# Performance work log

Hardware: AMD Instinct MI355X
Metric: run time of the kernel (lower is better)

The kernel has to match this reference:

```python
import jax, jax.numpy as jnp
import numpy as np

GRID_NUM = 3  # pykan 'grid' (number of intervals)
K = 3         # spline order

def bspline_basis(x, grid, k):
    # Cox-de Boor recursion, matching pykan B_batch with a shared extended grid.
    # x: (N, Din); grid: (G,) extended grid with G = GRID_NUM + 2*k + 1
    x = x[..., None]  # (N, Din, 1)
    B = ((x >= grid[:-1]) & (x < grid[1:])).astype(x.dtype)  # (N, Din, G-1)
    for p in range(1, k + 1):
        left = (x - grid[:-(p + 1)]) / (grid[p:-1] - grid[:-(p + 1)])
        right = (grid[p + 1:] - x) / (grid[p + 1:] - grid[1:-p])
        B = left * B[..., :-1] + right * B[..., 1:]
    return B  # (N, Din, GRID_NUM + k)

def setup_inputs() -> dict:
    key = jax.random.key(0)
    k1, k2, k3 = jax.random.split(key, 3)
    Bsz, S, Din, Dout = 4, 2048, 768, 768
    x = jax.random.normal(k1, (Bsz, S, Din), dtype=jnp.float32)
    # noise-scale-like init for spline coefficients (noise_scale=0.1)
    coef = (0.1 / GRID_NUM) * jax.random.normal(k2, (Dout, Din, GRID_NUM + K), dtype=jnp.float32)
    inv_sqrt_in = np.float32(1.0 / np.sqrt(Din))
    scale_base = inv_sqrt_in + 0.1 * inv_sqrt_in * jax.random.normal(k3, (Dout, Din), dtype=jnp.float32)
    scale_sp = jnp.ones((Dout, Din), dtype=jnp.float32)
    bias = jnp.zeros((Dout,), dtype=jnp.float32)
    return {"x": x, "coef": coef, "scale_base": scale_base, "scale_sp": scale_sp, "bias": bias}

def reference(x, coef, scale_base, scale_sp, bias):
    # x: (B, S, Din) -> flatten tokens as the original module does
    Bsz, S, Din = x.shape
    xf = x.reshape(-1, Din)  # (N, Din)
    # extended grid: linspace(-1,1,GRID_NUM+1) extended by K points each side (h = 2/GRID_NUM)
    h = 2.0 / GRID_NUM
    grid = jnp.arange(-K, GRID_NUM + K + 1, dtype=x.dtype) * h - 1.0  # (GRID_NUM + 2K + 1,)
    basis = bspline_basis(xf, grid, K)  # (N, Din, GRID_NUM+K)
    # per-edge activation: scale_base*silu(x) + scale_sp*spline(x); mask==1; symbolic branch==0
    base = jax.nn.silu(xf) @ scale_base.T  # (N, Dout)
    spline = jnp.einsum('nim,oim->no', basis, scale_sp[:, :, None] * coef)  # (N, Dout)
    out = base + spline + bias  # bias from pykan biases[l].weight
    return out.reshape(Bsz, S, -1)
```

## Files before the change

kernel.cpp:

```cpp
#include <hip/hip_runtime.h>
#include <hip/hip_bf16.h>


typedef _Float16 f16;
typedef __attribute__((ext_vector_type(8))) _Float16 f16x8;
typedef __attribute__((ext_vector_type(4))) float f32x4;

#define NTOK 8192
#define DIN 768
#define DOUT 768
#define KAUG 5376
#define BM 128
#define BN 96
#define BK 32
#define KSPLIT 2
#define KSEG (KAUG / KSPLIT)
#define KT (KSEG / BK)

#define A_BLOCKS 3072
#define W_BLOCKS 288
#define Z_BLOCKS 1536

typedef __attribute__((address_space(1))) void gvoid;
typedef __attribute__((address_space(3))) void lvoid;

__global__ __launch_bounds__(256) void build_all(const float* __restrict__ x,
                                                 const float* __restrict__ sb,
                                                 const float* __restrict__ ssp,
                                                 const float* __restrict__ coef,
                                                 f16* __restrict__ Aa,
                                                 f16* __restrict__ Wa,
                                                 float* __restrict__ out) {
  const int b = blockIdx.x;
  if (b < A_BLOCKS) {
    const int t = b * 256 + threadIdx.x;
    const int n = t / 96;
    const int i8 = (t - n * 96) * 8;

    const float4* xp = (const float4*)(x + (size_t)n * DIN + i8);
    float4 va = xp[0], vb = xp[1];
    float xv[8] = {va.x, va.y, va.z, va.w, vb.x, vb.y, vb.z, vb.w};

    f16x8 sil;
    f16x8 Bv[6];
#pragma unroll
    for (int e = 0; e < 8; ++e) {
      const float v = xv[e];
      sil[e] = (f16)__fdividef(v, 1.0f + __expf(-v));

      const float s = (v + 1.0f) * 1.5f + 3.0f;
      const float fi = floorf(s);
      const int i0 = (int)fi;
      const float u = s - fi;
      const float um = 1.0f - u;
      const float u2 = u * u, u3 = u2 * u;
      const float w0 = um * um * um * (1.0f / 6.0f);
      const float w1 = (3.0f * u3 - 6.0f * u2 + 4.0f) * (1.0f / 6.0f);
      const float w2 = (-3.0f * u3 + 3.0f * u2 + 3.0f * u + 1.0f) * (1.0f / 6.0f);
      const float w3 = u3 * (1.0f / 6.0f);
#pragma unroll
      for (int m = 0; m < 6; ++m) {
        const int d = m - i0 + 3;
        float w = (d == 0) ? w0 : (d == 1) ? w1 : (d == 2) ? w2 : (d == 3) ? w3 : 0.0f;
        Bv[m][e] = (f16)w;
      }
    }

    const size_t base = (size_t)n * KAUG + i8;
    *(f16x8*)&Aa[base] = sil;
#pragma unroll
    for (int m = 0; m < 6; ++m) *(f16x8*)&Aa[base + (size_t)(m + 1) * DIN] = Bv[m];
  } else if (b < A_BLOCKS + W_BLOCKS) {
    const int t = (b - A_BLOCKS) * 256 + threadIdx.x;
    const int o = t / 96;
    const int i8 = (t - o * 96) * 8;
    const size_t idx = (size_t)o * DIN + i8;

    float bb[8], sp[8], cf[48];
    *(float4*)&bb[0] = ((const float4*)(sb + idx))[0];
    *(float4*)&bb[4] = ((const float4*)(sb + idx))[1];
    *(float4*)&sp[0] = ((const float4*)(ssp + idx))[0];
    *(float4*)&sp[4] = ((const float4*)(ssp + idx))[1];
#pragma unroll
    for (int v = 0; v < 12; ++v) *(float4*)&cf[v * 4] = ((const float4*)(coef + idx * 6))[v];

    f16x8 ch0;
    f16x8 chm[6];
#pragma unroll
    for (int e = 0; e < 8; ++e) {
      ch0[e] = (f16)bb[e];
#pragma unroll
      for (int m = 0; m < 6; ++m) chm[m][e] = (f16)(sp[e] * cf[e * 6 + m]);
    }
    const size_t base = (size_t)o * KAUG + i8;
    *(f16x8*)&Wa[base] = ch0;
#pragma unroll
    for (int m = 0; m < 6; ++m) *(f16x8*)&Wa[base + (size_t)(m + 1) * DIN] = chm[m];
  } else {
    const int t = (b - A_BLOCKS - W_BLOCKS) * 256 + threadIdx.x;
    float4* o4 = (float4*)out;
    const float4 z = {0.f, 0.f, 0.f, 0.f};
#pragma unroll
    for (int s = 0; s < 4; ++s) o4[(size_t)t * 4 + s] = z;
  }
}

__global__ __launch_bounds__(256, 4) void kan_gemm(const f16* __restrict__ A,
                                                   const f16* __restrict__ W,
                                                   const float* __restrict__ bias,
                                                   float* __restrict__ out) {
  __shared__ alignas(16) f16 As[2][BM * BK];
  __shared__ alignas(16) f16 Bs[2][BN * BK];

  const int bid = blockIdx.x;
  const int xcd = bid & 7;
  const int slot = bid >> 3;
  const int mb = ((slot & 7) << 3) + xcd;
  const int rest = slot >> 3;
  const int nb = rest & 7;
  const int ks = rest >> 3;
  const int m0 = mb * BM;
  const int n0 = nb * BN;
  const size_t kbase = (size_t)ks * KSEG;

  const int tid = threadIdx.x;
  const int wave = tid >> 6;
  const int lane = tid & 63;
  const int wm = (wave >> 1) * 64;
  const int wn = (wave & 1) * 48;
  const int r = lane & 15;
  const int q = lane >> 4;

  f32x4 acc[4][3] = {};

  const int c0 = wave * 64 + lane;
  const int rowA0 = c0 >> 2, kq0 = c0 & 3;
  const int c1 = c0 + 256;
  const int rowA1 = c1 >> 2, kq1 = c1 & 3;

  const f16* gA0 = A + (size_t)(m0 + rowA0) * KAUG + kbase + kq0 * 8;
  const f16* gA1 = A + (size_t)(m0 + rowA1) * KAUG + kbase + kq1 * 8;
  const f16* gB0 = W + (size_t)(n0 + rowA0) * KAUG + kbase + kq0 * 8;
  const f16* gB1 = W + (size_t)(n0 + rowA1) * KAUG + kbase + kq1 * 8;

  const int woff = wave * 512;

  auto stage = [&](int buf, int kt) {
    const int koff = kt * BK;
    __builtin_amdgcn_global_load_lds((gvoid*)(gA0 + koff), (lvoid*)(&As[buf][woff]), 16, 0, 0);
    __builtin_amdgcn_global_load_lds((gvoid*)(gA1 + koff), (lvoid*)(&As[buf][woff + 2048]), 16, 0, 0);
    __builtin_amdgcn_global_load_lds((gvoid*)(gB0 + koff), (lvoid*)(&Bs[buf][woff]), 16, 0, 0);
    if (wave < 2)
      __builtin_amdgcn_global_load_lds((gvoid*)(gB1 + koff), (lvoid*)(&Bs[buf][woff + 2048]), 16, 0, 0);
  };

  stage(0, 0);

  for (int kt = 0; kt < KT; ++kt) {
    const int buf = kt & 1;
    __syncthreads();
    if (kt + 1 < KT) stage(buf ^ 1, kt + 1);

    f16x8 af[4], bf[3];
#pragma unroll
    for (int mi = 0; mi < 4; ++mi)
      af[mi] = *(const f16x8*)&As[buf][(wm + mi * 16 + r) * BK + q * 8];
#pragma unroll
    for (int ni = 0; ni < 3; ++ni)
      bf[ni] = *(const f16x8*)&Bs[buf][(wn + ni * 16 + r) * BK + q * 8];
#pragma unroll
    for (int mi = 0; mi < 4; ++mi)
#pragma unroll
      for (int ni = 0; ni < 3; ++ni)
        acc[mi][ni] =
            __builtin_amdgcn_mfma_f32_16x16x32_f16(af[mi], bf[ni], acc[mi][ni], 0, 0, 0);
  }

#pragma unroll
  for (int ni = 0; ni < 3; ++ni) {
    const int gcol = n0 + wn + ni * 16 + r;
    const float badd = (ks == 0) ? bias[gcol] : 0.0f;
#pragma unroll
    for (int mi = 0; mi < 4; ++mi) {
#pragma unroll
      for (int rg = 0; rg < 4; ++rg) {
        const int grow = m0 + wm + mi * 16 + q * 4 + rg;
        atomicAdd(&out[(size_t)grow * DOUT + gcol], acc[mi][ni][rg] + badd);
      }
    }
  }
}

extern "C" void kernel_launch(void* const* d_in, const int* in_sizes, int n_in,
                              void* d_out, int out_size, void* d_ws, size_t ws_size,
                              hipStream_t stream) {
  const float* x = (const float*)d_in[0];
  const float* coef = (const float*)d_in[1];
  const float* scale_base = (const float*)d_in[2];
  const float* scale_sp = (const float*)d_in[3];
  const float* bias = (const float*)d_in[4];
  float* out = (float*)d_out;

  f16* Aa = (f16*)d_ws;
  f16* Wa = (f16*)((char*)d_ws + (size_t)NTOK * KAUG * 2);

  build_all<<<A_BLOCKS + W_BLOCKS + Z_BLOCKS, 256, 0, stream>>>(x, scale_base, scale_sp,
                                                                coef, Aa, Wa, out);
  kan_gemm<<<8 * 128, 256, 0, stream>>>(Aa, Wa, bias, out);
}
```

Before: 228.6 us.

## Fuse activation basis construction into GEMM, drop materialized A matrix

Basis and SiLU features are now computed on the fly from x inside the GEMM and written straight to LDS, so the large fp16 augmented A matrix no longer goes out to global memory and back. The GEMM tile grows to 128x128, and the K split changes to two halves over the input dimension, each covering all seven feature channels. This removes most of the global memory traffic but puts the per-element spline math on the GEMM critical path. The loop is single-buffered with several syncs per iteration and 2 blocks per CU, so load/compute overlap and occupancy may drop.

```diff
diff --git a/kernel.cpp b/kernel.cpp
--- a/kernel.cpp
+++ b/kernel.cpp
@@ -11,43 +11,118 @@
 #define DOUT 768
 #define KAUG 5376
 #define BM 128
-#define BN 96
-#define BK 32
-#define KSPLIT 2
-#define KSEG (KAUG / KSPLIT)
-#define KT (KSEG / BK)
-
-#define A_BLOCKS 3072
+#define BN 128
+#define IB 32
+#define ISEG 384
+#define NIB 12
+
+#define ASTRIDE 40
+#define ASLICE (128 * ASTRIDE)
+#define BSLICE (128 * 32)
+
 #define W_BLOCKS 288
 #define Z_BLOCKS 1536
 
 typedef __attribute__((address_space(1))) void gvoid;
 typedef __attribute__((address_space(3))) void lvoid;
 
-__global__ __launch_bounds__(256) void build_all(const float* __restrict__ x,
-                                                 const float* __restrict__ sb,
-                                                 const float* __restrict__ ssp,
-                                                 const float* __restrict__ coef,
-                                                 f16* __restrict__ Aa,
-                                                 f16* __restrict__ Wa,
-                                                 float* __restrict__ out) {
+__global__ __launch_bounds__(256) void prep(const float* __restrict__ sb,
+                                            const float* __restrict__ ssp,
+                                            const float* __restrict__ coef,
+                                            f16* __restrict__ Wa,
+                                            float* __restrict__ out) {
   const int b = blockIdx.x;
-  if (b < A_BLOCKS) {
+  if (b < W_BLOCKS) {
     const int t = b * 256 + threadIdx.x;
-    const int n = t / 96;
-    const int i8 = (t - n * 96) * 8;
-
-    const float4* xp = (const float4*)(x + (size_t)n * DIN + i8);
-    float4 va = xp[0], vb = xp[1];
-    float xv[8] = {va.x, va.y, va.z, va.w, vb.x, vb.y, vb.z, vb.w};
-
-    f16x8 sil;
-    f16x8 Bv[6];
+    const int o = t / 96;
+    const int i8 = (t - o * 96) * 8;
+    const size_t idx = (size_t)o * DIN + i8;
+
+    float bb[8], sp[8], cf[48];
+    *(float4*)&bb[0] = ((const float4*)(sb + idx))[0];
+    *(float4*)&bb[4] = ((const float4*)(sb + idx))[1];
+    *(float4*)&sp[0] = ((const float4*)(ssp + idx))[0];
+    *(float4*)&sp[4] = ((const float4*)(ssp + idx))[1];
+#pragma unroll
+    for (int v = 0; v < 12; ++v) *(float4*)&cf[v * 4] = ((const float4*)(coef + idx * 6))[v];
+
+    f16x8 ch0, chm[6];
 #pragma unroll
     for (int e = 0; e < 8; ++e) {
+      ch0[e] = (f16)bb[e];
+#pragma unroll
+      for (int m = 0; m < 6; ++m) chm[m][e] = (f16)(sp[e] * cf[e * 6 + m]);
+    }
+    const size_t base = (size_t)o * KAUG + i8;
+    *(f16x8*)&Wa[base] = ch0;
+#pragma unroll
+    for (int m = 0; m < 6; ++m) *(f16x8*)&Wa[base + (size_t)(m + 1) * DIN] = chm[m];
+  } else {
+    const int t = (b - W_BLOCKS) * 256 + threadIdx.x;
+    float4* o4 = (float4*)out;
+    const float4 z = {0.f, 0.f, 0.f, 0.f};
+#pragma unroll
+    for (int s = 0; s < 4; ++s) o4[(size_t)t * 4 + s] = z;
+  }
+}
+
+__global__ __launch_bounds__(256, 2) void kan_fused(const float* __restrict__ x,
+                                                    const f16* __restrict__ Wa,
+                                                    const float* __restrict__ bias,
+                                                    float* __restrict__ out) {
+  __shared__ alignas(16) f16 As[4 * ASLICE];
+  __shared__ alignas(16) f16 Bs[4 * BSLICE];
+
+  const int bid = blockIdx.x;
+  const int xcd = bid & 7;
+  const int slot = bid >> 3;
+  const int mb = ((slot & 7) << 3) + xcd;
+  const int rest = slot >> 3;
+  const int nb = rest % 6;
+  const int ks = rest / 6;
+  const int m0 = mb * BM;
+  const int n0 = nb * BN;
+  const int ibase = ks * ISEG;
+
+  const int tid = threadIdx.x;
+  const int wave = tid >> 6;
+  const int lane = tid & 63;
+  const int wm = (wave >> 1) * 64;
+  const int wn = (wave & 1) * 64;
+  const int r = lane & 15;
+  const int q = lane >> 4;
+
+  const int xrow = tid >> 1;
+  const int ih = (tid & 1) * 16;
+  const float* xptr = x + (size_t)(m0 + xrow) * DIN + ibase + ih;
+  const int arow_off = xrow * ASTRIDE + ih;
+
+  const int c0 = wave * 64 + lane;
+  const int c1 = c0 + 256;
+  const f16* gB0 = Wa + (size_t)(n0 + (c0 >> 2)) * KAUG + ibase + (c0 & 3) * 8;
+  const f16* gB1 = Wa + (size_t)(n0 + (c1 >> 2)) * KAUG + ibase + (c1 & 3) * 8;
+  const int boff = wave * 512;
+
+  f32x4 acc[4][4] = {};
+
+  float4 xa[4];
+  xa[0] = ((const float4*)xptr)[0];
+  xa[1] = ((const float4*)xptr)[1];
+  xa[2] = ((const float4*)xptr)[2];
+  xa[3] = ((const float4*)xptr)[3];
+
+  for (int it = 0; it < NIB; ++it) {
+    float xv[16];
+    *(float4*)&xv[0] = xa[0];
+    *(float4*)&xv[4] = xa[1];
+    *(float4*)&xv[8] = xa[2];
+    *(float4*)&xv[12] = xa[3];
+
+    f16x8 chv[7][2];
+#pragma unroll
+    for (int e = 0; e < 16; ++e) {
       const float v = xv[e];
-      sil[e] = (f16)__fdividef(v, 1.0f + __expf(-v));
-
+      const float sil = __fdividef(v, 1.0f + __expf(-v));
       const float s = (v + 1.0f) * 1.5f + 3.0f;
       const float fi = floorf(s);
       const int i0 = (int)fi;
@@ -58,126 +133,79 @@
       const float w1 = (3.0f * u3 - 6.0f * u2 + 4.0f) * (1.0f / 6.0f);
       const float w2 = (-3.0f * u3 + 3.0f * u2 + 3.0f * u + 1.0f) * (1.0f / 6.0f);
       const float w3 = u3 * (1.0f / 6.0f);
+      chv[0][e >> 3][e & 7] = (f16)sil;
 #pragma unroll
       for (int m = 0; m < 6; ++m) {
         const int d = m - i0 + 3;
-        float w = (d == 0) ? w0 : (d == 1) ? w1 : (d == 2) ? w2 : (d == 3) ? w3 : 0.0f;
-        Bv[m][e] = (f16)w;
+        const float w = (d == 0) ? w0 : (d == 1) ? w1 : (d == 2) ? w2 : (d == 3) ? w3 : 0.0f;
+        chv[1 + m][e >> 3][e & 7] = (f16)w;
       }
     }
 
-    const size_t base = (size_t)n * KAUG + i8;
-    *(f16x8*)&Aa[base] = sil;
-#pragma unroll
-    for (int m = 0; m < 6; ++m) *(f16x8*)&Aa[base + (size_t)(m + 1) * DIN] = Bv[m];
-  } else if (b < A_BLOCKS + W_BLOCKS) {
-    const int t = (b - A_BLOCKS) * 256 + threadIdx.x;
-    const int o = t / 96;
-    const int i8 = (t - o * 96) * 8;
-    const size_t idx = (size_t)o * DIN + i8;
-
-    float bb[8], sp[8], cf[48];
-    *(float4*)&bb[0] = ((const float4*)(sb + idx))[0];
-    *(float4*)&bb[4] = ((const float4*)(sb + idx))[1];
-    *(float4*)&sp[0] = ((const float4*)(ssp + idx))[0];
-    *(float4*)&sp[4] = ((const float4*)(ssp + idx))[1];
-#pragma unroll
-    for (int v = 0; v < 12; ++v) *(float4*)&cf[v * 4] = ((const float4*)(coef + idx * 6))[v];
-
-    f16x8 ch0;
-    f16x8 chm[6];
-#pragma unroll
-    for (int e = 0; e < 8; ++e) {
-      ch0[e] = (f16)bb[e];
-#pragma unroll
-      for (int m = 0; m < 6; ++m) chm[m][e] = (f16)(sp[e] * cf[e * 6 + m]);
-    }
-    const size_t base = (size_t)o * KAUG + i8;
-    *(f16x8*)&Wa[base] = ch0;
-#pragma unroll
-    for (int m = 0; m < 6; ++m) *(f16x8*)&Wa[base + (size_t)(m + 1) * DIN] = chm[m];
-  } else {
-    const int t = (b - A_BLOCKS - W_BLOCKS) * 256 + threadIdx.x;
-    float4* o4 = (float4*)out;
-    const float4 z = {0.f, 0.f, 0.f, 0.f};
-#pragma unroll
-    for (int s = 0; s < 4; ++s) o4[(size_t)t * 4 + s] = z;
+#pragma unroll
+    for (int c = 0; c < 4; ++c) {
+      *(f16x8*)&As[c * ASLICE + arow_off] = chv[c][0];
+      *(f16x8*)&As[c * ASLICE + arow_off + 8] = chv[c][1];
+      const size_t gk = (size_t)c * DIN + it * IB;
+      __builtin_amdgcn_global_load_lds((gvoid*)(gB0 + gk), (lvoid*)(&Bs[c * BSLICE + boff]), 16, 0, 0);
+      __builtin_amdgcn_global_load_lds((gvoid*)(gB1 + gk), (lvoid*)(&Bs[c * BSLICE + boff + 2048]), 16, 0, 0);
+    }
+    __syncthreads();
+
+    if (it + 1 < NIB) {
+      const float* xn = xptr + (it + 1) * IB;
+      xa[0] = ((const float4*)xn)[0];
+      xa[1] = ((const float4*)xn)[1];
+      xa[2] = ((const float4*)xn)[2];
+      xa[3] = ((const float4*)xn)[3];
+    }
+#pragma unroll
+    for (int c = 0; c < 4; ++c) {
+      f16x8 af[4], bf[4];
+#pragma unroll
+      for (int mi = 0; mi < 4; ++mi)
+        af[mi] = *(const f16x8*)&As[c * ASLICE + (wm + mi * 16 + r) * ASTRIDE + q * 8];
+#pragma unroll
+      for (int ni = 0; ni < 4; ++ni)
+        bf[ni] = *(const f16x8*)&Bs[c * BSLICE + (wn + ni * 16 + r) * 32 + q * 8];
+#pragma unroll
+      for (int mi = 0; mi < 4; ++mi)
+#pragma unroll
+        for (int ni = 0; ni < 4; ++ni)
+          acc[mi][ni] = __builtin_amdgcn_mfma_f32_16x16x32_f16(af[mi], bf[ni], acc[mi][ni], 0, 0, 0);
+    }
+    __syncthreads();
+
+#pragma unroll
+    for (int c = 0; c < 3; ++c) {
+      *(f16x8*)&As[c * ASLICE + arow_off] = chv[4 + c][0];
+      *(f16x8*)&As[c * ASLICE + arow_off + 8] = chv[4 + c][1];
+      const size_t gk = (size_t)(4 + c) * DIN + it * IB;
+      __builtin_amdgcn_global_load_lds((gvoid*)(gB0 + gk), (lvoid*)(&Bs[c * BSLICE + boff]), 16, 0, 0);
+      __builtin_amdgcn_global_load_lds((gvoid*)(gB1 + gk), (lvoid*)(&Bs[c * BSLICE + boff + 2048]), 16, 0, 0);
+    }
+    __syncthreads();
+
+#pragma unroll
+    for (int c = 0; c < 3; ++c) {
+      f16x8 af[4], bf[4];
+#pragma unroll
+      for (int mi = 0; mi < 4; ++mi)
+        af[mi] = *(const f16x8*)&As[c * ASLICE + (wm + mi * 16 + r) * ASTRIDE + q * 8];
+#pragma unroll
+      for (int ni = 0; ni < 4; ++ni)
+        bf[ni] = *(const f16x8*)&Bs[c * BSLICE + (wn + ni * 16 + r) * 32 + q * 8];
+#pragma unroll
+      for (int mi = 0; mi < 4; ++mi)
+#pragma unroll
+        for (int ni = 0; ni < 4; ++ni)
+          acc[mi][ni] = __builtin_amdgcn_mfma_f32_16x16x32_f16(af[mi], bf[ni], acc[mi][ni], 0, 0, 0);
+    }
+    __syncthreads();
   }
-}
-
-__global__ __launch_bounds__(256, 4) void kan_gemm(const f16* __restrict__ A,
-                                                   const f16* __restrict__ W,
-                                                   const float* __restrict__ bias,
-                                                   float* __restrict__ out) {
-  __shared__ alignas(16) f16 As[2][BM * BK];
-  __shared__ alignas(16) f16 Bs[2][BN * BK];
-
-  const int bid = blockIdx.x;
-  const int xcd = bid & 7;
-  const int slot = bid >> 3;
-  const int mb = ((slot & 7) << 3) + xcd;
-  const int rest = slot >> 3;
-  const int nb = rest & 7;
-  const int ks = rest >> 3;
-  const int m0 = mb * BM;
-  const int n0 = nb * BN;
-  const size_t kbase = (size_t)ks * KSEG;
-
-  const int tid = threadIdx.x;
-  const int wave = tid >> 6;
-  const int lane = tid & 63;
-  const int wm = (wave >> 1) * 64;
-  const int wn = (wave & 1) * 48;
-  const int r = lane & 15;
-  const int q = lane >> 4;
-
-  f32x4 acc[4][3] = {};
-
-  const int c0 = wave * 64 + lane;
-  const int rowA0 = c0 >> 2, kq0 = c0 & 3;
-  const int c1 = c0 + 256;
-  const int rowA1 = c1 >> 2, kq1 = c1 & 3;
-
-  const f16* gA0 = A + (size_t)(m0 + rowA0) * KAUG + kbase + kq0 * 8;
-  const f16* gA1 = A + (size_t)(m0 + rowA1) * KAUG + kbase + kq1 * 8;
-  const f16* gB0 = W + (size_t)(n0 + rowA0) * KAUG + kbase + kq0 * 8;
-  const f16* gB1 = W + (size_t)(n0 + rowA1) * KAUG + kbase + kq1 * 8;
-
-  const int woff = wave * 512;
-
-  auto stage = [&](int buf, int kt) {
-    const int koff = kt * BK;
-    __builtin_amdgcn_global_load_lds((gvoid*)(gA0 + koff), (lvoid*)(&As[buf][woff]), 16, 0, 0);
-    __builtin_amdgcn_global_load_lds((gvoid*)(gA1 + koff), (lvoid*)(&As[buf][woff + 2048]), 16, 0, 0);
-    __builtin_amdgcn_global_load_lds((gvoid*)(gB0 + koff), (lvoid*)(&Bs[buf][woff]), 16, 0, 0);
-    if (wave < 2)
-      __builtin_amdgcn_global_load_lds((gvoid*)(gB1 + koff), (lvoid*)(&Bs[buf][woff + 2048]), 16, 0, 0);
-  };
-
-  stage(0, 0);
-
-  for (int kt = 0; kt < KT; ++kt) {
-    const int buf = kt & 1;
-    __syncthreads();
-    if (kt + 1 < KT) stage(buf ^ 1, kt + 1);
-
-    f16x8 af[4], bf[3];
-#pragma unroll
-    for (int mi = 0; mi < 4; ++mi)
-      af[mi] = *(const f16x8*)&As[buf][(wm + mi * 16 + r) * BK + q * 8];
-#pragma unroll
-    for (int ni = 0; ni < 3; ++ni)
-      bf[ni] = *(const f16x8*)&Bs[buf][(wn + ni * 16 + r) * BK + q * 8];
-#pragma unroll
-    for (int mi = 0; mi < 4; ++mi)
-#pragma unroll
-      for (int ni = 0; ni < 3; ++ni)
-        acc[mi][ni] =
-            __builtin_amdgcn_mfma_f32_16x16x32_f16(af[mi], bf[ni], acc[mi][ni], 0, 0, 0);
-  }
-
-#pragma unroll
-  for (int ni = 0; ni < 3; ++ni) {
+
+#pragma unroll
+  for (int ni = 0; ni < 4; ++ni) {
     const int gcol = n0 + wn + ni * 16 + r;
     const float badd = (ks == 0) ? bias[gcol] : 0.0f;
 #pragma unroll
@@ -201,10 +229,8 @@
   const float* bias = (const float*)d_in[4];
   float* out = (float*)d_out;
 
-  f16* Aa = (f16*)d_ws;
-  f16* Wa = (f16*)((char*)d_ws + (size_t)NTOK * KAUG * 2);
-
-  build_all<<<A_BLOCKS + W_BLOCKS + Z_BLOCKS, 256, 0, stream>>>(x, scale_base, scale_sp,
-                                                                coef, Aa, Wa, out);
-  kan_gemm<<<8 * 128, 256, 0, stream>>>(Aa, Wa, bias, out);
+  f16* Wa = (f16*)d_ws;
+
+  prep<<<W_BLOCKS + Z_BLOCKS, 256, 0, stream>>>(scale_base, scale_sp, coef, Wa, out);
+  kan_fused<<<768, 256, 0, stream>>>(x, Wa, bias, out);
 }
```

After: 466.6 us. 104% more time.

## Pre-swizzle operands into MFMA fragment layout and load directly to registers

Applied to the files above, without the earlier changes.

The build kernel now writes the augmented A and W matrices in a fragment-major layout, so each lane's 16-byte MFMA operand sits contiguously per 16-row block and k-step. The GEMM drops LDS staging and barriers entirely. Each wave instead loads its fragments straight from global memory into registers, with a two-step software prefetch. Tiles change to 128x128 per block with 4x4 MFMA tiles per wave, giving 768 blocks with a 2-way k-split. This removes LDS traffic and synchronisation but loses cross-wave operand sharing, relies on L2 for reuse, and raises register pressure.

```diff
diff --git a/kernel.cpp b/kernel.cpp
--- a/kernel.cpp
+++ b/kernel.cpp
@@ -10,19 +10,16 @@
 #define DIN 768
 #define DOUT 768
 #define KAUG 5376
-#define BM 128
-#define BN 96
-#define BK 32
-#define KSPLIT 2
-#define KSEG (KAUG / KSPLIT)
-#define KT (KSEG / BK)
+#define NKT 168
+#define KHALF 84
 
 #define A_BLOCKS 3072
 #define W_BLOCKS 288
 #define Z_BLOCKS 1536
 
-typedef __attribute__((address_space(1))) void gvoid;
-typedef __attribute__((address_space(3))) void lvoid;
+__device__ __forceinline__ size_t fragoff(int rb, int kt, int lane) {
+  return (((size_t)rb * NKT + kt) * 64 + lane) * 8;
+}
 
 __global__ __launch_bounds__(256) void build_all(const float* __restrict__ x,
                                                  const float* __restrict__ sb,
@@ -34,20 +31,18 @@
   const int b = blockIdx.x;
   if (b < A_BLOCKS) {
     const int t = b * 256 + threadIdx.x;
-    const int n = t / 96;
-    const int i8 = (t - n * 96) * 8;
-
-    const float4* xp = (const float4*)(x + (size_t)n * DIN + i8);
+    const int row = t / 96;
+    const int i8 = (t - row * 96) * 8;
+
+    const float4* xp = (const float4*)(x + (size_t)row * DIN + i8);
     float4 va = xp[0], vb = xp[1];
     float xv[8] = {va.x, va.y, va.z, va.w, vb.x, vb.y, vb.z, vb.w};
 
-    f16x8 sil;
-    f16x8 Bv[6];
+    f16x8 ch[7];
 #pragma unroll
     for (int e = 0; e < 8; ++e) {
       const float v = xv[e];
-      sil[e] = (f16)__fdividef(v, 1.0f + __expf(-v));
-
+      ch[0][e] = (f16)__fdividef(v, 1.0f + __expf(-v));
       const float s = (v + 1.0f) * 1.5f + 3.0f;
       const float fi = floorf(s);
       const int i0 = (int)fi;
@@ -61,15 +56,20 @@
 #pragma unroll
       for (int m = 0; m < 6; ++m) {
         const int d = m - i0 + 3;
-        float w = (d == 0) ? w0 : (d == 1) ? w1 : (d == 2) ? w2 : (d == 3) ? w3 : 0.0f;
-        Bv[m][e] = (f16)w;
+        const float w = (d == 0) ? w0 : (d == 1) ? w1 : (d == 2) ? w2 : (d == 3) ? w3 : 0.0f;
+        ch[1 + m][e] = (f16)w;
       }
     }
 
-    const size_t base = (size_t)n * KAUG + i8;
-    *(f16x8*)&Aa[base] = sil;
-#pragma unroll
-    for (int m = 0; m < 6; ++m) *(f16x8*)&Aa[base + (size_t)(m + 1) * DIN] = Bv[m];
+    const int rb = row >> 4;
+    const int rl = row & 15;
+#pragma unroll
+    for (int c = 0; c < 7; ++c) {
+      const int k = c * DIN + i8;
+      const int kt = k >> 5;
+      const int lane = ((k >> 3) & 3) * 16 + rl;
+      *(f16x8*)&Aa[fragoff(rb, kt, lane)] = ch[c];
+    }
   } else if (b < A_BLOCKS + W_BLOCKS) {
     const int t = (b - A_BLOCKS) * 256 + threadIdx.x;
     const int o = t / 96;
@@ -84,18 +84,23 @@
 #pragma unroll
     for (int v = 0; v < 12; ++v) *(float4*)&cf[v * 4] = ((const float4*)(coef + idx * 6))[v];
 
-    f16x8 ch0;
-    f16x8 chm[6];
+    f16x8 ch[7];
 #pragma unroll
     for (int e = 0; e < 8; ++e) {
-      ch0[e] = (f16)bb[e];
-#pragma unroll
-      for (int m = 0; m < 6; ++m) chm[m][e] = (f16)(sp[e] * cf[e * 6 + m]);
-    }
-    const size_t base = (size_t)o * KAUG + i8;
-    *(f16x8*)&Wa[base] = ch0;
-#pragma unroll
-    for (int m = 0; m < 6; ++m) *(f16x8*)&Wa[base + (size_t)(m + 1) * DIN] = chm[m];
+      ch[0][e] = (f16)bb[e];
+#pragma unroll
+      for (int m = 0; m < 6; ++m) ch[1 + m][e] = (f16)(sp[e] * cf[e * 6 + m]);
+    }
+
+    const int rb = o >> 4;
+    const int rl = o & 15;
+#pragma unroll
+    for (int c = 0; c < 7; ++c) {
+      const int k = c * DIN + i8;
+      const int kt = k >> 5;
+      const int lane = ((k >> 3) & 3) * 16 + rl;
+      *(f16x8*)&Wa[fragoff(rb, kt, lane)] = ch[c];
+    }
   } else {
     const int t = (b - A_BLOCKS - W_BLOCKS) * 256 + threadIdx.x;
     float4* o4 = (float4*)out;
@@ -105,86 +110,75 @@
   }
 }
 
-__global__ __launch_bounds__(256, 4) void kan_gemm(const f16* __restrict__ A,
-                                                   const f16* __restrict__ W,
-                                                   const float* __restrict__ bias,
-                                                   float* __restrict__ out) {
-  __shared__ alignas(16) f16 As[2][BM * BK];
-  __shared__ alignas(16) f16 Bs[2][BN * BK];
-
+__global__ __launch_bounds__(256, 3) void kan_rgemm(const f16* __restrict__ A,
+                                                    const f16* __restrict__ W,
+                                                    const float* __restrict__ bias,
+                                                    float* __restrict__ out) {
   const int bid = blockIdx.x;
   const int xcd = bid & 7;
   const int slot = bid >> 3;
   const int mb = ((slot & 7) << 3) + xcd;
   const int rest = slot >> 3;
-  const int nb = rest & 7;
-  const int ks = rest >> 3;
-  const int m0 = mb * BM;
-  const int n0 = nb * BN;
-  const size_t kbase = (size_t)ks * KSEG;
+  const int nb = rest % 6;
+  const int ks = rest / 6;
 
   const int tid = threadIdx.x;
   const int wave = tid >> 6;
   const int lane = tid & 63;
-  const int wm = (wave >> 1) * 64;
-  const int wn = (wave & 1) * 48;
+  const int k0 = ks * KHALF;
+
+  const int rb_base = mb * 8 + (wave >> 1) * 4;
+  const int cb_base = nb * 8 + (wave & 1) * 4;
+
+  const f16* pa[4];
+  const f16* pb[4];
+#pragma unroll
+  for (int mi = 0; mi < 4; ++mi) pa[mi] = A + fragoff(rb_base + mi, k0, lane);
+#pragma unroll
+  for (int ni = 0; ni < 4; ++ni) pb[ni] = W + fragoff(cb_base + ni, k0, lane);
+
+  f32x4 acc[4][4] = {};
+
+  f16x8 a0[4], b0[4], a1[4], b1[4];
+#pragma unroll
+  for (int mi = 0; mi < 4; ++mi) a0[mi] = *(const f16x8*)(pa[mi]);
+#pragma unroll
+  for (int ni = 0; ni < 4; ++ni) b0[ni] = *(const f16x8*)(pb[ni]);
+
+  for (int kk = 0; kk < KHALF; kk += 2) {
+#pragma unroll
+    for (int mi = 0; mi < 4; ++mi) a1[mi] = *(const f16x8*)(pa[mi] + (kk + 1) * 512);
+#pragma unroll
+    for (int ni = 0; ni < 4; ++ni) b1[ni] = *(const f16x8*)(pb[ni] + (kk + 1) * 512);
+#pragma unroll
+    for (int mi = 0; mi < 4; ++mi)
+#pragma unroll
+      for (int ni = 0; ni < 4; ++ni)
+        acc[mi][ni] = __builtin_amdgcn_mfma_f32_16x16x32_f16(a0[mi], b0[ni], acc[mi][ni], 0, 0, 0);
+    if (kk + 2 < KHALF) {
+#pragma unroll
+      for (int mi = 0; mi < 4; ++mi) a0[mi] = *(const f16x8*)(pa[mi] + (kk + 2) * 512);
+#pragma unroll
+      for (int ni = 0; ni < 4; ++ni) b0[ni] = *(const f16x8*)(pb[ni] + (kk + 2) * 512);
+    }
+#pragma unroll
+    for (int mi = 0; mi < 4; ++mi)
+#pragma unroll
+      for (int ni = 0; ni < 4; ++ni)
+        acc[mi][ni] = __builtin_amdgcn_mfma_f32_16x16x32_f16(a1[mi], b1[ni], acc[mi][ni], 0, 0, 0);
+  }
+
   const int r = lane & 15;
   const int q = lane >> 4;
-
-  f32x4 acc[4][3] = {};
-
-  const int c0 = wave * 64 + lane;
-  const int rowA0 = c0 >> 2, kq0 = c0 & 3;
-  const int c1 = c0 + 256;
-  const int rowA1 = c1 >> 2, kq1 = c1 & 3;
-
-  const f16* gA0 = A + (size_t)(m0 + rowA0) * KAUG + kbase + kq0 * 8;
-  const f16* gA1 = A + (size_t)(m0 + rowA1) * KAUG + kbase + kq1 * 8;
-  const f16* gB0 = W + (size_t)(n0 + rowA0) * KAUG + kbase + kq0 * 8;
-  const f16* gB1 = W + (size_t)(n0 + rowA1) * KAUG + kbase + kq1 * 8;
-
-  const int woff = wave * 512;
-
-  auto stage = [&](int buf, int kt) {
-    const int koff = kt * BK;
-    __builtin_amdgcn_global_load_lds((gvoid*)(gA0 + koff), (lvoid*)(&As[buf][woff]), 16, 0, 0);
-    __builtin_amdgcn_global_load_lds((gvoid*)(gA1 + koff), (lvoid*)(&As[buf][woff + 2048]), 16, 0, 0);
-    __builtin_amdgcn_global_load_lds((gvoid*)(gB0 + koff), (lvoid*)(&Bs[buf][woff]), 16, 0, 0);
-    if (wave < 2)
-      __builtin_amdgcn_global_load_lds((gvoid*)(gB1 + koff), (lvoid*)(&Bs[buf][woff + 2048]), 16, 0, 0);
-  };
-
-  stage(0, 0);
-
-  for (int kt = 0; kt < KT; ++kt) {
-    const int buf = kt & 1;
-    __syncthreads();
-    if (kt + 1 < KT) stage(buf ^ 1, kt + 1);
-
-    f16x8 af[4], bf[3];
-#pragma unroll
-    for (int mi = 0; mi < 4; ++mi)
-      af[mi] = *(const f16x8*)&As[buf][(wm + mi * 16 + r) * BK + q * 8];
-#pragma unroll
-    for (int ni = 0; ni < 3; ++ni)
-      bf[ni] = *(const f16x8*)&Bs[buf][(wn + ni * 16 + r) * BK + q * 8];
-#pragma unroll
-    for (int mi = 0; mi < 4; ++mi)
-#pragma unroll
-      for (int ni = 0; ni < 3; ++ni)
-        acc[mi][ni] =
-            __builtin_amdgcn_mfma_f32_16x16x32_f16(af[mi], bf[ni], acc[mi][ni], 0, 0, 0);
-  }
-
-#pragma unroll
-  for (int ni = 0; ni < 3; ++ni) {
-    const int gcol = n0 + wn + ni * 16 + r;
+#pragma unroll
+  for (int ni = 0; ni < 4; ++ni) {
+    const int gcol = (cb_base + ni) * 16 + r;
     const float badd = (ks == 0) ? bias[gcol] : 0.0f;
 #pragma unroll
     for (int mi = 0; mi < 4; ++mi) {
 #pragma unroll
       for (int rg = 0; rg < 4; ++rg) {
-        const int grow = m0 + wm + mi * 16 + q * 4 + rg;
+        const int grow = (rb_base + mi) * 16 + q * 4 + rg;
         atomicAdd(&out[(size_t)grow * DOUT + gcol], acc[mi][ni][rg] + badd);
       }
     }
@@ -206,5 +200,5 @@
 
   build_all<<<A_BLOCKS + W_BLOCKS + Z_BLOCKS, 256, 0, stream>>>(x, scale_base, scale_sp,
                                                                 coef, Aa, Wa, out);
-  kan_gemm<<<8 * 128, 256, 0, stream>>>(Aa, Wa, bias, out);
-}
+  kan_rgemm<<<768, 256, 0, stream>>>(Aa, Wa, bias, out);
+}
```

Result: slower. 254.5 us (+11.3%).
